# Performance work log

Hardware: AMD Instinct MI355X
Metric: run time of the kernel (lower is better)

Reference implementation:

```python
import jax, jax.numpy as jnp
import numpy as np
import math

B, C, H, W = 512, 64, 8, 8
E, NH, MEM = 64, 8, 8          # embed_dim, num_heads, mem_n
HD = E // NH                   # head_dim
THD = H * W * HD               # tot_head_dim = 512
AMB = 5.0                      # attn_mask_b
LN_EPS = 1e-5


def conv2d(x, w, b):
    y = jax.lax.conv_general_dilated(x, w, (1, 1), 'SAME',
                                     dimension_numbers=('NCHW', 'OIHW', 'NCHW'))
    return y + b[None, :, None, None]


def setup_inputs() -> dict:
    key = jax.random.key(0)
    ks = jax.random.split(key, 14)
    r = lambda k, s, sc=1.0: jax.random.normal(k, s, dtype=jnp.float32) * sc
    return {
        'input': r(ks[0], (B, C, H, W)),
        'h_cur': r(ks[1], (B, E, H, W)),
        'c_cur': r(ks[2], (B, E, H, W)),
        'concat_k': r(ks[3], (B, MEM, NH, THD)),
        'concat_v': r(ks[4], (B, MEM, NH, THD)),
        'attn_mask': jax.random.randint(ks[5], (B * NH, 1, MEM), 0, 2).astype(bool),
        'conv_w': r(ks[6], (5 * E, C + E, 3, 3), 0.05),
        'conv_b': jnp.zeros((5 * E,), jnp.float32),
        'proj_w': r(ks[7], (3 * E, C, 3, 3), 0.05),
        'proj_b': jnp.zeros((3 * E,), jnp.float32),
        'out_w': r(ks[8], (E, E, 3, 3), 0.05),
        'out_b': jnp.zeros((E,), jnp.float32),
        'ln_w': jnp.ones((E, H, W), jnp.float32),
        'ln_b': jnp.zeros((E, H, W), jnp.float32),
        'pos_w': r(ks[9], (MEM, H * W * E), 0.02),
        'pos_b': jax.random.uniform(ks[10], (MEM, NH), jnp.float32, -0.1, 0.1),
    }


def _cell(input, h_cur, c_cur, concat_k, concat_v, attn_mask,
          conv_w, conv_b, proj_w, proj_b, out_w, out_b, ln_w, ln_b, pos_w, pos_b):
    # ConvLSTM gates
    combined = jnp.concatenate([input, h_cur], axis=1)          # [B, C+E, H, W]
    cc = conv2d(combined, conv_w, conv_b)                       # [B, 5E, H, W]
    cc_i, cc_f, cc_o, cc_g, cc_a = jnp.split(cc, 5, axis=1)
    i = jax.nn.sigmoid(cc_i)
    f = jax.nn.sigmoid(cc_f)
    o = jax.nn.sigmoid(cc_o)
    g = jnp.tanh(cc_g)
    a = jax.nn.sigmoid(cc_a)
    c_next = f * c_cur + i * g

    # attention over growing memory
    kqv = conv2d(input, proj_w, proj_b)                         # [B, 3E, H, W]
    k, q, v = jnp.split(kqv, 3, axis=1)
    # [B, E, H, W] -> [B*NH, 1, THD] (contiguous split of E into NH heads)
    resh = lambda x: x.reshape(B * NH, 1, THD)
    k, q, v = resh(k), resh(q), resh(v)
    q_scaled = q / math.sqrt(THD)

    # prior memory: [B, MEM, NH, THD] -> [B*NH, MEM-1, THD]
    def mem_resh(m):
        return jnp.transpose(m[:, 1:], (1, 0, 2, 3)).reshape(MEM - 1, B * NH, THD).transpose(1, 0, 2)
    k_full = jnp.concatenate([mem_resh(concat_k), k], axis=1)   # [B*NH, MEM, THD]
    v_full = jnp.concatenate([mem_resh(concat_v), v], axis=1)

    # learned positional key offsets / score biases
    pos_w_e = jnp.broadcast_to(pos_w[:, None, :], (MEM, B, H * W * E)) \
                 .reshape(MEM, B * NH, THD).transpose(1, 0, 2)  # [B*NH, MEM, THD]
    pos_b_e = jnp.broadcast_to(pos_b[:, None, :], (MEM, B, NH)) \
                 .reshape(MEM, B * NH).T                        # [B*NH, MEM]
    k_full = k_full + pos_w_e

    # additive mask: -inf where masked, last slot forced to +attn_mask_b
    mask = jnp.where(attn_mask, -jnp.inf, 0.0).astype(q.dtype)  # [B*NH, 1, MEM]
    mask = mask.at[:, :, -1].set(AMB)

    scores = mask + jnp.einsum('bqd,bkd->bqk', q_scaled, k_full) + pos_b_e[:, None, :]
    w = jax.nn.softmax(scores, axis=-1)                         # [B*NH, 1, MEM]
    attn = jnp.einsum('bqk,bkd->bqd', w, v_full)                # [B*NH, 1, THD]
    attn = attn.reshape(B, E, H, W)

    out = conv2d(attn, out_w, out_b) + input[:, :E]
    # LayerNorm over (E, H, W)
    mu = jnp.mean(out, axis=(1, 2, 3), keepdims=True)
    var = jnp.mean((out - mu) ** 2, axis=(1, 2, 3), keepdims=True)
    out = (out - mu) / jnp.sqrt(var + LN_EPS) * ln_w[None] + ln_b[None]

    c_next = c_next + a * jnp.tanh(out)
    h_next = o * jnp.tanh(c_next)

    ret = lambda m: m.transpose(1, 0, 2).reshape(MEM, B, NH, THD).transpose(1, 0, 2, 3)
    return h_next, c_next, ret(k_full), ret(v_full)


def reference(input, h_cur, c_cur, concat_k, concat_v, attn_mask,
              conv_w, conv_b, proj_w, proj_b, out_w, out_b, ln_w, ln_b, pos_w, pos_b):
    return _cell(input, h_cur, c_cur, concat_k, concat_v, attn_mask,
                 conv_w, conv_b, proj_w, proj_b, out_w, out_b, ln_w, ln_b, pos_w, pos_b)
```

## Files before the change

kernel.cpp:

```cpp
#include <hip/hip_runtime.h>

typedef short short8 __attribute__((ext_vector_type(8)));
typedef __bf16 bf16x8 __attribute__((ext_vector_type(8)));
typedef float f32x4 __attribute__((ext_vector_type(4)));
typedef short s16x4 __attribute__((ext_vector_type(4)));
typedef unsigned u32x4 __attribute__((ext_vector_type(4)));

__device__ __forceinline__ short f2bf(float f) {
  unsigned u = __builtin_bit_cast(unsigned, f);
  u = (u + 0x7FFFu + ((u >> 16) & 1u)) >> 16;
  return (short)u;
}
__device__ __forceinline__ f32x4 mfma16(short8 a, short8 b, f32x4 c) {
  return __builtin_amdgcn_mfma_f32_16x16x32_bf16(
      __builtin_bit_cast(bf16x8, a), __builtin_bit_cast(bf16x8, b), c, 0, 0, 0);
}
__device__ __forceinline__ float sigm(float x) { return 1.0f / (1.0f + __expf(-x)); }
__device__ __forceinline__ float ftanh(float x) {
  return 1.0f - 2.0f / (1.0f + __expf(2.0f * x));
}
__device__ __forceinline__ f32x4 ntld4(const float* p) {
  return __builtin_nontemporal_load((const f32x4*)p);
}
__device__ __forceinline__ void ntst4(float* p, f32x4 v) {
  __builtin_nontemporal_store(v, (f32x4*)p);
}

__global__ void pack_w(const float* __restrict__ w1, const float* __restrict__ w2,
                       const float* __restrict__ w3, short* __restrict__ out) {
  int e = blockIdx.x * 256 + threadIdx.x;
  if (e < 46080) {
    int kb8 = e / 320, n = e % 320;
    short8 v;
#pragma unroll
    for (int j = 0; j < 8; ++j) {
      int k = kb8 * 8 + j;
      int tap = k >> 7, ci = k & 127;
      v[j] = f2bf(w1[(n * 128 + ci) * 9 + tap]);
    }
    *(short8*)&out[e * 8] = v;
    return;
  }
  e -= 46080;
  if (e < 13824) {
    int kb8 = e / 192, n = e % 192;
    short8 v;
#pragma unroll
    for (int j = 0; j < 8; ++j) {
      int k = kb8 * 8 + j;
      int tap = k >> 6, ci = k & 63;
      v[j] = f2bf(w2[(n * 64 + ci) * 9 + tap]);
    }
    *(short8*)&out[(46080 + e) * 8] = v;
    return;
  }
  e -= 13824;
  {
    int kb8 = e / 64, n = e % 64;
    short8 v;
#pragma unroll
    for (int j = 0; j < 8; ++j) {
      int k = kb8 * 8 + j;
      int tap = k >> 6, ci = k & 63;
      v[j] = f2bf(w3[(n * 64 + ci) * 9 + tap]);
    }
    *(short8*)&out[(46080 + 13824 + e) * 8] = v;
  }
}

__launch_bounds__(512, 4)
__global__ void mid_k(const float* __restrict__ input, const float* __restrict__ h_cur,
                      const float* __restrict__ c_cur, const float* __restrict__ ck,
                      const float* __restrict__ cv, const int* __restrict__ amask,
                      const float* __restrict__ conv_b, const float* __restrict__ proj_b,
                      const float* __restrict__ pos_w, const float* __restrict__ pos_b,
                      const short* __restrict__ pk1, const short* __restrict__ pk2,
                      float* __restrict__ o_k, float* __restrict__ o_v,
                      short* __restrict__ ws_attn, float* __restrict__ ws_ct,
                      unsigned* __restrict__ ws_oa) {
  __shared__ short comb[12800];
  __shared__ float Xb[4160];
  __shared__ float Vx[4160];
  __shared__ float sc_lds[8];
  float* combf = (float*)comb;
  unsigned* Xbu = (unsigned*)Xb;

  const int tid = threadIdx.x;
  const int wave = tid >> 6, lane = tid & 63;
  const int col = lane & 15, g4 = lane >> 4;
  const int wc = wave >> 1, wm = wave & 1;
  const int ch = wc * 16 + col;

  if (blockIdx.x < 512) {
    const int b = blockIdx.x;
    const int hd = wave;
    const int d0 = lane * 4, d1 = (lane + 64) * 4;
    if (tid < 8) sc_lds[tid] = 0.f;

#pragma unroll
    for (int i = 0; i < 2; ++i) {
      int idx = (tid + 512 * i) * 4;
      int c = idx >> 6, p0 = idx & 63;
      f32x4 vi = *(const f32x4*)&input[b * 4096 + idx];
#pragma unroll
      for (int j = 0; j < 4; ++j) {
        int p = p0 + j;
        int pp = ((p >> 3) + 1) * 10 + (p & 7) + 1;
        comb[pp * 64 + ((c + pp * 8) & 63)] = f2bf(vi[j]);
      }
    }
    for (int i = tid; i < 2304; i += 512) {
      int pr = i >> 6, c = i & 63;
      int pp = (pr < 10) ? pr
               : (pr < 20) ? (80 + pr)
               : (pr < 28) ? ((pr - 19) * 10)
                           : ((pr - 27) * 10 + 9);
      comb[pp * 64 + c] = 0;
    }
    __syncthreads();

    f32x4 acc2[2][3];
#pragma unroll
    for (int m = 0; m < 2; ++m)
#pragma unroll
      for (int g = 0; g < 3; ++g) acc2[m][g] = (f32x4){0.f, 0.f, 0.f, 0.f};
    short8 bb2[3];
#pragma unroll
    for (int g = 0; g < 3; ++g)
      bb2[g] = *(const short8*)&pk2[((g4)*192 + g * 64 + ch) * 8];
    for (int s = 0; s < 18; ++s) {
      short8 bbn[3];
      if (s < 17) {
        int kb8 = (s + 1) * 4 + g4;
#pragma unroll
        for (int g = 0; g < 3; ++g)
          bbn[g] = *(const short8*)&pk2[(kb8 * 192 + g * 64 + ch) * 8];
      }
      int tap = s >> 1, cib = s & 1;
      int kh = tap / 3, kw = tap % 3;
      short8 a[2];
#pragma unroll
      for (int m = 0; m < 2; ++m) {
        int p = (wm * 2 + m) * 16 + col;
        int pp = ((p >> 3) + kh) * 10 + (p & 7) + kw;
        int slot = (cib * 32 + g4 * 8 + pp * 8) & 63;
        a[m] = *(const short8*)&comb[pp * 64 + slot];
      }
#pragma unroll
      for (int m = 0; m < 2; ++m)
#pragma unroll
        for (int g = 0; g < 3; ++g) acc2[m][g] = mfma16(a[m], bb2[g], acc2[m][g]);
      if (s < 17) {
#pragma unroll
        for (int g = 0; g < 3; ++g) bb2[g] = bbn[g];
      }
    }

    float kreg[8], qreg[8], vreg[8], part7 = 0.f;
    {
      float pb0 = proj_b[ch], pb1 = proj_b[64 + ch], pb2 = proj_b[128 + ch];
      const float rsq = 0.044194173824159216f;
#pragma unroll
      for (int m = 0; m < 2; ++m)
#pragma unroll
        for (int r = 0; r < 4; ++r) {
          int p = (wm * 2 + m) * 16 + g4 * 4 + r;
          float kf = acc2[m][0][r] + pb0 + pos_w[7 * 4096 + ch * 64 + p];
          float qf = (acc2[m][1][r] + pb1) * rsq;
          float vf = acc2[m][2][r] + pb2;
          kreg[m * 4 + r] = kf;
          qreg[m * 4 + r] = qf;
          vreg[m * 4 + r] = vf;
          part7 = fmaf(qf, kf, part7);
        }
    }
    atomicAdd(&sc_lds[ch >> 3], part7);

    f32x4 kk0[7], kk1[7];
#pragma unroll
    for (int m = 0; m < 7; ++m) {
      const float* kp = ck + ((size_t)((b * 8 + m + 1) * 8 + hd)) * 512;
      kk0[m] = ntld4(kp + d0);
      kk1[m] = ntld4(kp + d1);
    }

    __syncthreads();

#pragma unroll
    for (int m = 0; m < 2; ++m)
#pragma unroll
      for (int r = 0; r < 4; ++r) {
        int p = (wm * 2 + m) * 16 + g4 * 4 + r;
        combf[ch * 65 + p] = kreg[m * 4 + r];
        Xb[ch * 65 + p] = qreg[m * 4 + r];
        Vx[ch * 65 + p] = vreg[m * 4 + r];
      }
    __syncthreads();

    const size_t base7 = (size_t)(b * 64 + 56) * 512;
#pragma unroll
    for (int i = 0; i < 2; ++i) {
      int idx = (tid + 512 * i) * 4;
      int c = idx >> 6, p0 = idx & 63;
      f32x4 kq, vq;
#pragma unroll
      for (int j = 0; j < 4; ++j) {
        kq[j] = combf[c * 65 + p0 + j];
        vq[j] = Vx[c * 65 + p0 + j];
      }
      ntst4(&o_k[base7 + idx], kq);
      ntst4(&o_v[base7 + idx], vq);
    }
    const int cs0 = d0 >> 6, po0 = d0 & 63, cs1 = d1 >> 6, po1 = d1 & 63;
    f32x4 q0, q1, v70, v71;
#pragma unroll
    for (int j = 0; j < 4; ++j) {
      q0[j] = Xb[(hd * 8 + cs0) * 65 + po0 + j];
      q1[j] = Xb[(hd * 8 + cs1) * 65 + po1 + j];
      v70[j] = Vx[(hd * 8 + cs0) * 65 + po0 + j];
      v71[j] = Vx[(hd * 8 + cs1) * 65 + po1 + j];
    }
    float sc7 = sc_lds[hd] + pos_b[7 * 8 + hd] + 5.0f;

    float scv[8];
    scv[7] = sc7;
#pragma unroll
    for (int m = 0; m < 7; ++m) {
      const float* pw = pos_w + m * 4096 + hd * 512;
      f32x4 k0 = kk0[m] + *(const f32x4*)&pw[d0];
      f32x4 k1 = kk1[m] + *(const f32x4*)&pw[d1];
      float* dst = o_k + ((size_t)((b * 8 + m) * 8 + hd)) * 512;
      ntst4(dst + d0, k0);
      ntst4(dst + d1, k1);
      float part = 0.f;
#pragma unroll
      for (int j = 0; j < 4; ++j) {
        part = fmaf(q0[j], k0[j], part);
        part = fmaf(q1[j], k1[j], part);
      }
#pragma unroll
      for (int off = 32; off >= 1; off >>= 1) part += __shfl_xor(part, off);
      float msk = amask[(b * 8 + hd) * 8 + m] ? -__builtin_inff() : 0.0f;
      scv[m] = part + pos_b[m * 8 + hd] + msk;
    }

    f32x4 vv0[7], vv1[7];
#pragma unroll
    for (int m = 0; m < 7; ++m) {
      const float* vp = cv + ((size_t)((b * 8 + m + 1) * 8 + hd)) * 512;
      vv0[m] = ntld4(vp + d0);
      vv1[m] = ntld4(vp + d1);
    }

    float mx = scv[0];
#pragma unroll
    for (int m = 1; m < 8; ++m) mx = fmaxf(mx, scv[m]);
    float w[8], s = 0.f;
#pragma unroll
    for (int m = 0; m < 8; ++m) {
      w[m] = __expf(scv[m] - mx);
      s += w[m];
    }
    float inv = 1.0f / s;
#pragma unroll
    for (int m = 0; m < 8; ++m) w[m] *= inv;

    f32x4 a0 = (f32x4){0.f, 0.f, 0.f, 0.f};
    f32x4 a1 = (f32x4){0.f, 0.f, 0.f, 0.f};
#pragma unroll
    for (int m = 0; m < 7; ++m) {
      float* dst = o_v + ((size_t)((b * 8 + m) * 8 + hd)) * 512;
      ntst4(dst + d0, vv0[m]);
      ntst4(dst + d1, vv1[m]);
      a0 += vv0[m] * w[m];
      a1 += vv1[m] * w[m];
    }
    a0 += v70 * w[7];
    a1 += v71 * w[7];

    s16x4 s0, s1;
#pragma unroll
    for (int j = 0; j < 4; ++j) {
      s0[j] = f2bf(a0[j]);
      s1[j] = f2bf(a1[j]);
    }
    *(s16x4*)&ws_attn[(size_t)b * 4096 + hd * 512 + d0] = s0;
    *(s16x4*)&ws_attn[(size_t)b * 4096 + hd * 512 + d1] = s1;
  } else {
    const int b = blockIdx.x - 512;
#pragma unroll
    for (int i = 0; i < 2; ++i) {
      int idx = (tid + 512 * i) * 4;
      int c = idx >> 6, p0 = idx & 63;
      f32x4 vi = *(const f32x4*)&input[b * 4096 + idx];
      f32x4 vh = *(const f32x4*)&h_cur[b * 4096 + idx];
      f32x4 vc = *(const f32x4*)&c_cur[b * 4096 + idx];
#pragma unroll
      for (int j = 0; j < 4; ++j) {
        int p = p0 + j;
        int pp = ((p >> 3) + 1) * 10 + (p & 7) + 1;
        comb[pp * 128 + ((c + pp * 8) & 127)] = f2bf(vi[j]);
        comb[pp * 128 + ((c + 64 + pp * 8) & 127)] = f2bf(vh[j]);
        Xb[c * 65 + p] = vc[j];
      }
    }
    for (int i = tid; i < 4608; i += 512) {
      int pr = i >> 7, c = i & 127;
      int pp = (pr < 10) ? pr
               : (pr < 20) ? (80 + pr)
               : (pr < 28) ? ((pr - 19) * 10)
                           : ((pr - 27) * 10 + 9);
      comb[pp * 128 + c] = 0;
    }
    __syncthreads();

    f32x4 acc1[2][5];
#pragma unroll
    for (int m = 0; m < 2; ++m)
#pragma unroll
      for (int g = 0; g < 5; ++g) acc1[m][g] = (f32x4){0.f, 0.f, 0.f, 0.f};
    short8 bb1[5];
#pragma unroll
    for (int g = 0; g < 5; ++g)
      bb1[g] = *(const short8*)&pk1[((g4)*320 + g * 64 + ch) * 8];
    for (int s = 0; s < 36; ++s) {
      short8 bbn[5];
      if (s < 35) {
        int kb8 = (s + 1) * 4 + g4;
#pragma unroll
        for (int g = 0; g < 5; ++g)
          bbn[g] = *(const short8*)&pk1[(kb8 * 320 + g * 64 + ch) * 8];
      }
      int tap = s >> 2, cib = s & 3;
      int kh = tap / 3, kw = tap % 3;
      short8 a[2];
#pragma unroll
      for (int m = 0; m < 2; ++m) {
        int p = (wm * 2 + m) * 16 + col;
        int pp = ((p >> 3) + kh) * 10 + (p & 7) + kw;
        int slot = (cib * 32 + g4 * 8 + pp * 8) & 127;
        a[m] = *(const short8*)&comb[pp * 128 + slot];
      }
#pragma unroll
      for (int m = 0; m < 2; ++m)
#pragma unroll
        for (int g = 0; g < 5; ++g) acc1[m][g] = mfma16(a[m], bb1[g], acc1[m][g]);
      if (s < 35) {
#pragma unroll
        for (int g = 0; g < 5; ++g) bb1[g] = bbn[g];
      }
    }

    float ctv[8];
    unsigned oav[8];
    {
      float bi0 = conv_b[ch], bi1 = conv_b[64 + ch], bi2 = conv_b[128 + ch];
      float bi3 = conv_b[192 + ch], bi4 = conv_b[256 + ch];
#pragma unroll
      for (int m = 0; m < 2; ++m)
#pragma unroll
        for (int r = 0; r < 4; ++r) {
          int p = (wm * 2 + m) * 16 + g4 * 4 + r;
          float iv = sigm(acc1[m][0][r] + bi0);
          float fv = sigm(acc1[m][1][r] + bi1);
          float ov = sigm(acc1[m][2][r] + bi2);
          float gv = ftanh(acc1[m][3][r] + bi3);
          float av = sigm(acc1[m][4][r] + bi4);
          ctv[m * 4 + r] = fv * Xb[ch * 65 + p] + iv * gv;
          oav[m * 4 + r] = ((unsigned)(unsigned short)f2bf(av) << 16) |
                           (unsigned)(unsigned short)f2bf(ov);
        }
    }
    __syncthreads();
#pragma unroll
    for (int m = 0; m < 2; ++m)
#pragma unroll
      for (int r = 0; r < 4; ++r) {
        int p = (wm * 2 + m) * 16 + g4 * 4 + r;
        combf[ch * 65 + p] = ctv[m * 4 + r];
        Xbu[ch * 65 + p] = oav[m * 4 + r];
      }
    __syncthreads();
#pragma unroll
    for (int i = 0; i < 2; ++i) {
      int idx = (tid + 512 * i) * 4;
      int c = idx >> 6, p0 = idx & 63;
      f32x4 cq;
      u32x4 oq;
#pragma unroll
      for (int j = 0; j < 4; ++j) {
        cq[j] = combf[c * 65 + p0 + j];
        oq[j] = Xbu[c * 65 + p0 + j];
      }
      *(f32x4*)&ws_ct[(size_t)b * 4096 + idx] = cq;
      *(u32x4*)&ws_oa[(size_t)b * 4096 + idx] = oq;
    }
  }
}

__launch_bounds__(512, 4)
__global__ void back_k(const float* __restrict__ input,
                       const short* __restrict__ ws_attn,
                       const float* __restrict__ ws_ct,
                       const unsigned* __restrict__ ws_oa,
                       const float* __restrict__ out_b,
                       const float* __restrict__ ln_w, const float* __restrict__ ln_b,
                       const short* __restrict__ pk3,
                       float* __restrict__ o_h, float* __restrict__ o_c) {
  __shared__ short comb[8320];
  __shared__ float Xb[4160];
  __shared__ float red[16];
  float* combf = (float*)comb;
  unsigned* Xbu = (unsigned*)Xb;

  const int b = blockIdx.x;
  const int tid = threadIdx.x;
  const int wave = tid >> 6, lane = tid & 63;
  const int col = lane & 15, g4 = lane >> 4;
  const int wc = wave >> 1, wm = wave & 1;
  const int ch = wc * 16 + col;

  f32x4 ctr[2];
  u32x4 oar[2];
#pragma unroll
  for (int i = 0; i < 2; ++i) {
    int idx = (tid + 512 * i) * 4;
    ctr[i] = *(const f32x4*)&ws_ct[(size_t)b * 4096 + idx];
    oar[i] = *(const u32x4*)&ws_oa[(size_t)b * 4096 + idx];
  }
#pragma unroll
  for (int i = 0; i < 2; ++i) {
    int idx = (tid + 512 * i) * 4;
    int c = idx >> 6, p0 = idx & 63;
    s16x4 av = *(const s16x4*)&ws_attn[(size_t)b * 4096 + idx];
    f32x4 vi = *(const f32x4*)&input[b * 4096 + idx];
#pragma unroll
    for (int j = 0; j < 4; ++j) {
      int p = p0 + j;
      int pp = ((p >> 3) + 1) * 10 + (p & 7) + 1;
      comb[pp * 64 + ((c + pp * 8) & 63)] = av[j];
      Xb[c * 65 + p] = vi[j];
    }
  }
  for (int i = tid; i < 2304; i += 512) {
    int pr = i >> 6, c = i & 63;
    int pp = (pr < 10) ? pr
             : (pr < 20) ? (80 + pr)
             : (pr < 28) ? ((pr - 19) * 10)
                         : ((pr - 27) * 10 + 9);
    comb[pp * 64 + c] = 0;
  }
  __syncthreads();

  f32x4 acc3[2];
  acc3[0] = (f32x4){0.f, 0.f, 0.f, 0.f};
  acc3[1] = (f32x4){0.f, 0.f, 0.f, 0.f};
  short8 bb3 = *(const short8*)&pk3[((g4)*64 + ch) * 8];
  for (int s = 0; s < 18; ++s) {
    short8 bbn;
    if (s < 17) {
      int kb8 = (s + 1) * 4 + g4;
      bbn = *(const short8*)&pk3[(kb8 * 64 + ch) * 8];
    }
    int tap = s >> 1, cib = s & 1;
    int kh = tap / 3, kw = tap % 3;
    short8 a[2];
#pragma unroll
    for (int m = 0; m < 2; ++m) {
      int p = (wm * 2 + m) * 16 + col;
      int pp = ((p >> 3) + kh) * 10 + (p & 7) + kw;
      int slot = (cib * 32 + g4 * 8 + pp * 8) & 63;
      a[m] = *(const short8*)&comb[pp * 64 + slot];
    }
#pragma unroll
    for (int m = 0; m < 2; ++m) acc3[m] = mfma16(a[m], bb3, acc3[m]);
    if (s < 17) bb3 = bbn;
  }

  float ov_[8], s1 = 0.f, s2 = 0.f;
  {
    float ob = out_b[ch];
#pragma unroll
    for (int m = 0; m < 2; ++m)
#pragma unroll
      for (int r = 0; r < 4; ++r) {
        int p = (wm * 2 + m) * 16 + g4 * 4 + r;
        float v = acc3[m][r] + ob + Xb[ch * 65 + p];
        ov_[m * 4 + r] = v;
        s1 += v;
        s2 += v * v;
      }
  }
#pragma unroll
  for (int off = 32; off >= 1; off >>= 1) {
    s1 += __shfl_xor(s1, off);
    s2 += __shfl_xor(s2, off);
  }
  if (lane == 0) { red[wave] = s1; red[8 + wave] = s2; }
  __syncthreads();
  float ts1 = 0.f, ts2 = 0.f;
#pragma unroll
  for (int w = 0; w < 8; ++w) { ts1 += red[w]; ts2 += red[8 + w]; }
  float mu = ts1 * (1.0f / 4096.0f);
  float var = ts2 * (1.0f / 4096.0f) - mu * mu;
  float rstd = rsqrtf(var + 1e-5f);

#pragma unroll
  for (int i = 0; i < 2; ++i) {
    int idx = (tid + 512 * i) * 4;
    int c = idx >> 6, p0 = idx & 63;
#pragma unroll
    for (int j = 0; j < 4; ++j) {
      combf[c * 65 + p0 + j] = ctr[i][j];
      Xbu[c * 65 + p0 + j] = oar[i][j];
    }
  }
  __syncthreads();

#pragma unroll
  for (int m = 0; m < 2; ++m)
#pragma unroll
    for (int r = 0; r < 4; ++r) {
      int p = (wm * 2 + m) * 16 + g4 * 4 + r;
      float ct = combf[ch * 65 + p];
      unsigned u = Xbu[ch * 65 + p];
      float og = __builtin_bit_cast(float, u << 16);
      float ag = __builtin_bit_cast(float, u & 0xffff0000u);
      float oln = (ov_[m * 4 + r] - mu) * rstd * ln_w[ch * 64 + p] + ln_b[ch * 64 + p];
      float cn = ct + ag * ftanh(oln);
      float hv = og * ftanh(cn);
      combf[ch * 65 + p] = hv;
      Xb[ch * 65 + p] = cn;
    }
  __syncthreads();
#pragma unroll
  for (int i = 0; i < 2; ++i) {
    int idx = (tid + 512 * i) * 4;
    int c = idx >> 6, p0 = idx & 63;
    f32x4 hq, cq;
#pragma unroll
    for (int j = 0; j < 4; ++j) {
      hq[j] = combf[c * 65 + p0 + j];
      cq[j] = Xb[c * 65 + p0 + j];
    }
    *(f32x4*)&o_h[b * 4096 + idx] = hq;
    *(f32x4*)&o_c[b * 4096 + idx] = cq;
  }
}

__launch_bounds__(512, 4)
__global__ void kqv_k(const float* __restrict__ input,
                      const float* __restrict__ proj_b,
                      const float* __restrict__ pos_w,
                      const short* __restrict__ pk2,
                      float* __restrict__ q_out, float* __restrict__ o_k,
                      float* __restrict__ o_v) {
  __shared__ short comb[6400];
  __shared__ float Xk[4160], Xq[4160], Xv[4160];
  const int b = blockIdx.x;
  const int tid = threadIdx.x;
  const int wave = tid >> 6, lane = tid & 63;
  const int col = lane & 15, g4 = lane >> 4;
  const int wc = wave >> 1, wm = wave & 1;
  const int ch = wc * 16 + col;
#pragma unroll
  for (int i = 0; i < 2; ++i) {
    int idx = (tid + 512 * i) * 4;
    int c = idx >> 6, p0 = idx & 63;
    f32x4 vi = *(const f32x4*)&input[b * 4096 + idx];
#pragma unroll
    for (int j = 0; j < 4; ++j) {
      int p = p0 + j;
      int pp = ((p >> 3) + 1) * 10 + (p & 7) + 1;
      comb[pp * 64 + ((c + pp * 8) & 63)] = f2bf(vi[j]);
    }
  }
  for (int i = tid; i < 2304; i += 512) {
    int pr = i >> 6, c = i & 63;
    int pp = (pr < 10) ? pr
             : (pr < 20) ? (80 + pr)
             : (pr < 28) ? ((pr - 19) * 10)
                         : ((pr - 27) * 10 + 9);
    comb[pp * 64 + c] = 0;
  }
  __syncthreads();
  f32x4 acc2[2][3];
#pragma unroll
  for (int m = 0; m < 2; ++m)
#pragma unroll
    for (int g = 0; g < 3; ++g) acc2[m][g] = (f32x4){0.f, 0.f, 0.f, 0.f};
  short8 bb2[3];
#pragma unroll
  for (int g = 0; g < 3; ++g)
    bb2[g] = *(const short8*)&pk2[((g4)*192 + g * 64 + ch) * 8];
  for (int s = 0; s < 18; ++s) {
    short8 bbn[3];
    if (s < 17) {
      int kb8 = (s + 1) * 4 + g4;
#pragma unroll
      for (int g = 0; g < 3; ++g)
        bbn[g] = *(const short8*)&pk2[(kb8 * 192 + g * 64 + ch) * 8];
    }
    int tap = s >> 1, cib = s & 1;
    int kh = tap / 3, kw = tap % 3;
    short8 a[2];
#pragma unroll
    for (int m = 0; m < 2; ++m) {
      int p = (wm * 2 + m) * 16 + col;
      int pp = ((p >> 3) + kh) * 10 + (p & 7) + kw;
      int slot = (cib * 32 + g4 * 8 + pp * 8) & 63;
      a[m] = *(const short8*)&comb[pp * 64 + slot];
    }
#pragma unroll
    for (int m = 0; m < 2; ++m)
#pragma unroll
      for (int g = 0; g < 3; ++g) acc2[m][g] = mfma16(a[m], bb2[g], acc2[m][g]);
    if (s < 17) {
#pragma unroll
      for (int g = 0; g < 3; ++g) bb2[g] = bbn[g];
    }
  }
  {
    float pb0 = proj_b[ch], pb1 = proj_b[64 + ch], pb2 = proj_b[128 + ch];
    const float rsq = 0.044194173824159216f;
#pragma unroll
    for (int m = 0; m < 2; ++m)
#pragma unroll
      for (int r = 0; r < 4; ++r) {
        int p = (wm * 2 + m) * 16 + g4 * 4 + r;
        Xk[ch * 65 + p] = acc2[m][0][r] + pb0 + pos_w[7 * 4096 + ch * 64 + p];
        Xq[ch * 65 + p] = (acc2[m][1][r] + pb1) * rsq;
        Xv[ch * 65 + p] = acc2[m][2][r] + pb2;
      }
  }
  __syncthreads();
  const size_t base7 = (size_t)(b * 64 + 56) * 512;
#pragma unroll
  for (int i = 0; i < 2; ++i) {
    int idx = (tid + 512 * i) * 4;
    int c = idx >> 6, p0 = idx & 63;
    f32x4 kq, qq, vq;
#pragma unroll
    for (int j = 0; j < 4; ++j) {
      kq[j] = Xk[c * 65 + p0 + j];
      qq[j] = Xq[c * 65 + p0 + j];
      vq[j] = Xv[c * 65 + p0 + j];
    }
    *(f32x4*)&o_k[base7 + idx] = kq;
    *(f32x4*)&q_out[(size_t)b * 4096 + idx] = qq;
    *(f32x4*)&o_v[base7 + idx] = vq;
  }
}

__launch_bounds__(64, 4)
__global__ void attn_k(const float* __restrict__ ck, const float* __restrict__ cv,
                       const int* __restrict__ amask,
                       const float* __restrict__ pos_w,
                       const float* __restrict__ pos_b,
                       const float* __restrict__ q_in,
                       float* __restrict__ o_k, float* __restrict__ o_v,
                       float* __restrict__ attn_out) {
  const int b = blockIdx.x >> 3;
  const int hd = blockIdx.x & 7;
  const int lane = threadIdx.x;
  const int d0 = lane * 4, d1 = (lane + 64) * 4;
  const float* qp = q_in + (size_t)b * 4096 + hd * 512;
  f32x4 q0 = *(const f32x4*)&qp[d0];
  f32x4 q1 = *(const f32x4*)&qp[d1];
  float sc[8];
#pragma unroll
  for (int m = 0; m < 7; ++m) {
    const float* kp = ck + ((size_t)((b * 8 + m + 1) * 8 + hd)) * 512;
    const float* pw = pos_w + m * 4096 + hd * 512;
    f32x4 k0 = ntld4(kp + d0) + *(const f32x4*)&pw[d0];
    f32x4 k1 = ntld4(kp + d1) + *(const f32x4*)&pw[d1];
    float* dst = o_k + ((size_t)((b * 8 + m) * 8 + hd)) * 512;
    ntst4(dst + d0, k0);
    ntst4(dst + d1, k1);
    float part = 0.f;
#pragma unroll
    for (int j = 0; j < 4; ++j) {
      part = fmaf(q0[j], k0[j], part);
      part = fmaf(q1[j], k1[j], part);
    }
#pragma unroll
    for (int off = 32; off >= 1; off >>= 1) part += __shfl_xor(part, off);
    float msk = amask[(b * 8 + hd) * 8 + m] ? -__builtin_inff() : 0.0f;
    sc[m] = part + pos_b[m * 8 + hd] + msk;
  }
  {
    const float* kp = o_k + ((size_t)((b * 8 + 7) * 8 + hd)) * 512;
    f32x4 k0 = *(const f32x4*)&kp[d0];
    f32x4 k1 = *(const f32x4*)&kp[d1];
    float part = 0.f;
#pragma unroll
    for (int j = 0; j < 4; ++j) {
      part = fmaf(q0[j], k0[j], part);
      part = fmaf(q1[j], k1[j], part);
    }
#pragma unroll
    for (int off = 32; off >= 1; off >>= 1) part += __shfl_xor(part, off);
    sc[7] = part + pos_b[7 * 8 + hd] + 5.0f;
  }
  float mx = sc[0];
#pragma unroll
  for (int m = 1; m < 8; ++m) mx = fmaxf(mx, sc[m]);
  float w[8], s = 0.f;
#pragma unroll
  for (int m = 0; m < 8; ++m) {
    w[m] = __expf(sc[m] - mx);
    s += w[m];
  }
  float inv = 1.0f / s;
#pragma unroll
  for (int m = 0; m < 8; ++m) w[m] *= inv;
  f32x4 a0 = (f32x4){0.f, 0.f, 0.f, 0.f};
  f32x4 a1 = (f32x4){0.f, 0.f, 0.f, 0.f};
#pragma unroll
  for (int m = 0; m < 7; ++m) {
    const float* vp = cv + ((size_t)((b * 8 + m + 1) * 8 + hd)) * 512;
    f32x4 v0 = ntld4(vp + d0);
    f32x4 v1 = ntld4(vp + d1);
    float* dst = o_v + ((size_t)((b * 8 + m) * 8 + hd)) * 512;
    ntst4(dst + d0, v0);
    ntst4(dst + d1, v1);
    a0 += v0 * w[m];
    a1 += v1 * w[m];
  }
  {
    const float* vp = o_v + ((size_t)((b * 8 + 7) * 8 + hd)) * 512;
    a0 += *(const f32x4*)&vp[d0] * w[7];
    a1 += *(const f32x4*)&vp[d1] * w[7];
  }
  float* ap = attn_out + (size_t)b * 4096 + hd * 512;
  *(f32x4*)&ap[d0] = a0;
  *(f32x4*)&ap[d1] = a1;
}

__launch_bounds__(512, 4)
__global__ void cell2_k(
    const float* __restrict__ input, const float* __restrict__ h_cur,
    const float* __restrict__ c_cur, const float* __restrict__ attn_in,
    const float* __restrict__ conv_b, const float* __restrict__ out_b,
    const float* __restrict__ ln_w, const float* __restrict__ ln_b,
    const short* __restrict__ pk1, const short* __restrict__ pk3,
    float* __restrict__ o_h, float* __restrict__ o_c) {
  __shared__ short comb[12800];
  __shared__ float Xb[4160];
  __shared__ float Qb[4160];
  __shared__ float Vb[4160];
  __shared__ float red[16];
  const int b = blockIdx.x;
  const int tid = threadIdx.x;
  const int wave = tid >> 6, lane = tid & 63;
  const int col = lane & 15, g4 = lane >> 4;
  const int wc = wave >> 1, wm = wave & 1;
  const int ch = wc * 16 + col;
#pragma unroll
  for (int i = 0; i < 2; ++i) {
    int idx = (tid + 512 * i) * 4;
    int c = idx >> 6, p0 = idx & 63;
    f32x4 vi = *(const f32x4*)&input[b * 4096 + idx];
    f32x4 vh = *(const f32x4*)&h_cur[b * 4096 + idx];
    f32x4 vc = *(const f32x4*)&c_cur[b * 4096 + idx];
#pragma unroll
    for (int j = 0; j < 4; ++j) {
      int p = p0 + j;
      int pp = ((p >> 3) + 1) * 10 + (p & 7) + 1;
      comb[pp * 128 + ((c + pp * 8) & 127)] = f2bf(vi[j]);
      comb[pp * 128 + ((c + 64 + pp * 8) & 127)] = f2bf(vh[j]);
      Xb[c * 65 + p] = vc[j];
    }
  }
  for (int i = tid; i < 4608; i += 512) {
    int pr = i >> 7, c = i & 127;
    int pp = (pr < 10) ? pr
             : (pr < 20) ? (80 + pr)
             : (pr < 28) ? ((pr - 19) * 10)
                         : ((pr - 27) * 10 + 9);
    comb[pp * 128 + c] = 0;
  }
  __syncthreads();
  f32x4 acc1[2][5];
#pragma unroll
  for (int m = 0; m < 2; ++m)
#pragma unroll
    for (int g = 0; g < 5; ++g) acc1[m][g] = (f32x4){0.f, 0.f, 0.f, 0.f};
  short8 bb1[5];
#pragma unroll
  for (int g = 0; g < 5; ++g)
    bb1[g] = *(const short8*)&pk1[((g4)*320 + g * 64 + ch) * 8];
  for (int s = 0; s < 36; ++s) {
    short8 bbn[5];
    if (s < 35) {
      int kb8 = (s + 1) * 4 + g4;
#pragma unroll
      for (int g = 0; g < 5; ++g)
        bbn[g] = *(const short8*)&pk1[(kb8 * 320 + g * 64 + ch) * 8];
    }
    int tap = s >> 2, cib = s & 3;
    int kh = tap / 3, kw = tap % 3;
    short8 a[2];
#pragma unroll
    for (int m = 0; m < 2; ++m) {
      int p = (wm * 2 + m) * 16 + col;
      int pp = ((p >> 3) + kh) * 10 + (p & 7) + kw;
      int slot = (cib * 32 + g4 * 8 + pp * 8) & 127;
      a[m] = *(const short8*)&comb[pp * 128 + slot];
    }
#pragma unroll
    for (int m = 0; m < 2; ++m)
#pragma unroll
      for (int g = 0; g < 5; ++g) acc1[m][g] = mfma16(a[m], bb1[g], acc1[m][g]);
    if (s < 35) {
#pragma unroll
      for (int g = 0; g < 5; ++g) bb1[g] = bbn[g];
    }
  }
  float ct_r[8], o_r[8], a_r[8];
  {
    float bi0 = conv_b[ch], bi1 = conv_b[64 + ch], bi2 = conv_b[128 + ch];
    float bi3 = conv_b[192 + ch], bi4 = conv_b[256 + ch];
#pragma unroll
    for (int m = 0; m < 2; ++m)
#pragma unroll
      for (int r = 0; r < 4; ++r) {
        int p = (wm * 2 + m) * 16 + g4 * 4 + r;
        float iv = sigm(acc1[m][0][r] + bi0);
        float fv = sigm(acc1[m][1][r] + bi1);
        float ov = sigm(acc1[m][2][r] + bi2);
        float gv = ftanh(acc1[m][3][r] + bi3);
        float av = sigm(acc1[m][4][r] + bi4);
        ct_r[m * 4 + r] = fv * Xb[ch * 65 + p] + iv * gv;
        o_r[m * 4 + r] = ov;
        a_r[m * 4 + r] = av;
      }
  }
  __syncthreads();
  {
    f32x4 av[2], iv[2];
#pragma unroll
    for (int i = 0; i < 2; ++i) {
      int idx = (tid + 512 * i) * 4;
      av[i] = *(const f32x4*)&attn_in[b * 4096 + idx];
      iv[i] = *(const f32x4*)&input[b * 4096 + idx];
    }
#pragma unroll
    for (int i = 0; i < 2; ++i) {
      int idx = (tid + 512 * i) * 4;
      int c = idx >> 6, p0 = idx & 63;
#pragma unroll
      for (int j = 0; j < 4; ++j) {
        int p = p0 + j;
        int pp = ((p >> 3) + 1) * 10 + (p & 7) + 1;
        comb[pp * 128 + ((c + pp * 8) & 127)] = f2bf(av[i][j]);
        Xb[c * 65 + p] = iv[i][j];
      }
    }
  }
  __syncthreads();
  f32x4 acc3[2];
  acc3[0] = (f32x4){0.f, 0.f, 0.f, 0.f};
  acc3[1] = (f32x4){0.f, 0.f, 0.f, 0.f};
  short8 bb3 = *(const short8*)&pk3[((g4)*64 + ch) * 8];
  for (int s = 0; s < 18; ++s) {
    short8 bbn;
    if (s < 17) {
      int kb8 = (s + 1) * 4 + g4;
      bbn = *(const short8*)&pk3[(kb8 * 64 + ch) * 8];
    }
    int tap = s >> 1, cib = s & 1;
    int kh = tap / 3, kw = tap % 3;
    short8 a[2];
#pragma unroll
    for (int m = 0; m < 2; ++m) {
      int p = (wm * 2 + m) * 16 + col;
      int pp = ((p >> 3) + kh) * 10 + (p & 7) + kw;
      int slot = (cib * 32 + g4 * 8 + pp * 8) & 127;
      a[m] = *(const short8*)&comb[pp * 128 + slot];
    }
#pragma unroll
    for (int m = 0; m < 2; ++m) acc3[m] = mfma16(a[m], bb3, acc3[m]);
    if (s < 17) bb3 = bbn;
  }
  float ov_[8], s1 = 0.f, s2 = 0.f;
  {
    float ob = out_b[ch];
#pragma unroll
    for (int m = 0; m < 2; ++m)
#pragma unroll
      for (int r = 0; r < 4; ++r) {
        int p = (wm * 2 + m) * 16 + g4 * 4 + r;
        float v = acc3[m][r] + ob + Xb[ch * 65 + p];
        ov_[m * 4 + r] = v;
        s1 += v;
        s2 += v * v;
      }
  }
#pragma unroll
  for (int off = 32; off >= 1; off >>= 1) {
    s1 += __shfl_xor(s1, off);
    s2 += __shfl_xor(s2, off);
  }
  if (lane == 0) { red[wave] = s1; red[8 + wave] = s2; }
  __syncthreads();
  float ts1 = 0.f, ts2 = 0.f;
#pragma unroll
  for (int w = 0; w < 8; ++w) { ts1 += red[w]; ts2 += red[8 + w]; }
  float mu = ts1 * (1.0f / 4096.0f);
  float var = ts2 * (1.0f / 4096.0f) - mu * mu;
  float rstd = rsqrtf(var + 1e-5f);
#pragma unroll
  for (int m = 0; m < 2; ++m)
#pragma unroll
    for (int r = 0; r < 4; ++r) {
      int p = (wm * 2 + m) * 16 + g4 * 4 + r;
      float oln = (ov_[m * 4 + r] - mu) * rstd * ln_w[ch * 64 + p] + ln_b[ch * 64 + p];
      float cn = ct_r[m * 4 + r] + a_r[m * 4 + r] * ftanh(oln);
      float hv = o_r[m * 4 + r] * ftanh(cn);
      Qb[ch * 65 + p] = hv;
      Vb[ch * 65 + p] = cn;
    }
  __syncthreads();
#pragma unroll
  for (int i = 0; i < 2; ++i) {
    int idx = (tid + 512 * i) * 4;
    int c = idx >> 6, p0 = idx & 63;
    f32x4 hv, cvv;
#pragma unroll
    for (int j = 0; j < 4; ++j) {
      hv[j] = Qb[c * 65 + p0 + j];
      cvv[j] = Vb[c * 65 + p0 + j];
    }
    *(f32x4*)&o_h[b * 4096 + idx] = hv;
    *(f32x4*)&o_c[b * 4096 + idx] = cvv;
  }
}

extern "C" void kernel_launch(void* const* d_in, const int* in_sizes, int n_in,
                              void* d_out, int out_size, void* d_ws, size_t ws_size,
                              hipStream_t stream) {
  (void)in_sizes; (void)n_in; (void)out_size;
  const float* input  = (const float*)d_in[0];
  const float* h_cur  = (const float*)d_in[1];
  const float* c_cur  = (const float*)d_in[2];
  const float* ck     = (const float*)d_in[3];
  const float* cv     = (const float*)d_in[4];
  const int*   amask  = (const int*)d_in[5];
  const float* conv_w = (const float*)d_in[6];
  const float* conv_b = (const float*)d_in[7];
  const float* proj_w = (const float*)d_in[8];
  const float* proj_b = (const float*)d_in[9];
  const float* out_w  = (const float*)d_in[10];
  const float* out_b  = (const float*)d_in[11];
  const float* ln_w   = (const float*)d_in[12];
  const float* ln_b   = (const float*)d_in[13];
  const float* pos_w  = (const float*)d_in[14];
  const float* pos_b  = (const float*)d_in[15];

  char* ws = (char*)d_ws;
  short* pk = (short*)ws;
  float* o_h = (float*)d_out;
  float* o_c = o_h + 2097152;
  float* o_k = o_h + 4194304;
  float* o_v = o_h + 20971520;

  pack_w<<<252, 256, 0, stream>>>(conv_w, proj_w, out_w, pk);

  if (ws_size >= (24u << 20)) {
    short* ws_attn = (short*)(ws + (2u << 20));
    float* ws_ct = (float*)(ws + (8u << 20));
    unsigned* ws_oa = (unsigned*)(ws + (16u << 20));
    mid_k<<<1024, 512, 0, stream>>>(input, h_cur, c_cur, ck, cv, amask,
                                    conv_b, proj_b, pos_w, pos_b,
                                    pk, pk + 368640,
                                    o_k, o_v, ws_attn, ws_ct, ws_oa);
    back_k<<<512, 512, 0, stream>>>(input, ws_attn, ws_ct, ws_oa,
                                    out_b, ln_w, ln_b, pk + 479232, o_h, o_c);
  } else {
    kqv_k<<<512, 512, 0, stream>>>(input, proj_b, pos_w, pk + 368640,
                                   o_h, o_k, o_v);
    attn_k<<<4096, 64, 0, stream>>>(ck, cv, amask, pos_w, pos_b, o_h,
                                    o_k, o_v, o_c);
    cell2_k<<<512, 512, 0, stream>>>(input, h_cur, c_cur, o_c,
                                     conv_b, out_b, ln_w, ln_b,
                                     pk, pk + 479232, o_h, o_c);
  }
}
```

Measured before the change: 106.0 us.

## Move V-weighted sum and V copy into tail kernel, pass softmax weights

The attention-weighted sum over V, and the copy of concat_v into the output, move from the mid kernel to the tail kernel. The mid kernel now writes only the normalized softmax weights per head to workspace, which lowers its register pressure and load traffic and balances work between the two kernels. Nontemporal loads are replaced with plain loads throughout, and the position-7 V store becomes a regular store so the tail kernel can read it back. The tail kernel then does extra global loads and scatters the bf16 attention result into LDS itself.

Result: faster. 99.34 us (-6.3%).

```diff
diff --git a/kernel.cpp b/kernel.cpp
--- a/kernel.cpp
+++ b/kernel.cpp
@@ -19,9 +19,7 @@
 __device__ __forceinline__ float ftanh(float x) {
   return 1.0f - 2.0f / (1.0f + __expf(2.0f * x));
 }
-__device__ __forceinline__ f32x4 ntld4(const float* p) {
-  return __builtin_nontemporal_load((const f32x4*)p);
-}
+__device__ __forceinline__ f32x4 ld4(const float* p) { return *(const f32x4*)p; }
 __device__ __forceinline__ void ntst4(float* p, f32x4 v) {
   __builtin_nontemporal_store(v, (f32x4*)p);
 }
@@ -69,15 +67,15 @@
 }
 
 __launch_bounds__(512, 4)
-__global__ void mid_k(const float* __restrict__ input, const float* __restrict__ h_cur,
-                      const float* __restrict__ c_cur, const float* __restrict__ ck,
-                      const float* __restrict__ cv, const int* __restrict__ amask,
-                      const float* __restrict__ conv_b, const float* __restrict__ proj_b,
-                      const float* __restrict__ pos_w, const float* __restrict__ pos_b,
-                      const short* __restrict__ pk1, const short* __restrict__ pk2,
-                      float* __restrict__ o_k, float* __restrict__ o_v,
-                      short* __restrict__ ws_attn, float* __restrict__ ws_ct,
-                      unsigned* __restrict__ ws_oa) {
+__global__ void mid2_k(const float* __restrict__ input, const float* __restrict__ h_cur,
+                       const float* __restrict__ c_cur, const float* __restrict__ ck,
+                       const int* __restrict__ amask,
+                       const float* __restrict__ conv_b, const float* __restrict__ proj_b,
+                       const float* __restrict__ pos_w, const float* __restrict__ pos_b,
+                       const short* __restrict__ pk1, const short* __restrict__ pk2,
+                       float* __restrict__ o_k, float* __restrict__ o_v,
+                       float* __restrict__ ws_wt, float* __restrict__ ws_ct,
+                       unsigned* __restrict__ ws_oa) {
   __shared__ short comb[12800];
   __shared__ float Xb[4160];
   __shared__ float Vx[4160];
@@ -101,7 +99,7 @@
     for (int i = 0; i < 2; ++i) {
       int idx = (tid + 512 * i) * 4;
       int c = idx >> 6, p0 = idx & 63;
-      f32x4 vi = *(const f32x4*)&input[b * 4096 + idx];
+      f32x4 vi = ld4(&input[b * 4096 + idx]);
 #pragma unroll
       for (int j = 0; j < 4; ++j) {
         int p = p0 + j;
@@ -176,12 +174,12 @@
     }
     atomicAdd(&sc_lds[ch >> 3], part7);
 
-    f32x4 kk0[7], kk1[7];
+    int msks[7];
+    float pbv[7];
 #pragma unroll
     for (int m = 0; m < 7; ++m) {
-      const float* kp = ck + ((size_t)((b * 8 + m + 1) * 8 + hd)) * 512;
-      kk0[m] = ntld4(kp + d0);
-      kk1[m] = ntld4(kp + d1);
+      msks[m] = amask[(b * 8 + hd) * 8 + m];
+      pbv[m] = pos_b[m * 8 + hd];
     }
 
     __syncthreads();
@@ -209,16 +207,14 @@
         vq[j] = Vx[c * 65 + p0 + j];
       }
       ntst4(&o_k[base7 + idx], kq);
-      ntst4(&o_v[base7 + idx], vq);
+      *(f32x4*)&o_v[base7 + idx] = vq;
     }
     const int cs0 = d0 >> 6, po0 = d0 & 63, cs1 = d1 >> 6, po1 = d1 & 63;
-    f32x4 q0, q1, v70, v71;
+    f32x4 q0, q1;
 #pragma unroll
     for (int j = 0; j < 4; ++j) {
       q0[j] = Xb[(hd * 8 + cs0) * 65 + po0 + j];
       q1[j] = Xb[(hd * 8 + cs1) * 65 + po1 + j];
-      v70[j] = Vx[(hd * 8 + cs0) * 65 + po0 + j];
-      v71[j] = Vx[(hd * 8 + cs1) * 65 + po1 + j];
     }
     float sc7 = sc_lds[hd] + pos_b[7 * 8 + hd] + 5.0f;
 
@@ -226,9 +222,10 @@
     scv[7] = sc7;
 #pragma unroll
     for (int m = 0; m < 7; ++m) {
+      const float* kp = ck + ((size_t)((b * 8 + m + 1) * 8 + hd)) * 512;
       const float* pw = pos_w + m * 4096 + hd * 512;
-      f32x4 k0 = kk0[m] + *(const f32x4*)&pw[d0];
-      f32x4 k1 = kk1[m] + *(const f32x4*)&pw[d1];
+      f32x4 k0 = ld4(kp + d0) + ld4(pw + d0);
+      f32x4 k1 = ld4(kp + d1) + ld4(pw + d1);
       float* dst = o_k + ((size_t)((b * 8 + m) * 8 + hd)) * 512;
       ntst4(dst + d0, k0);
       ntst4(dst + d1, k1);
@@ -240,16 +237,7 @@
       }
 #pragma unroll
       for (int off = 32; off >= 1; off >>= 1) part += __shfl_xor(part, off);
-      float msk = amask[(b * 8 + hd) * 8 + m] ? -__builtin_inff() : 0.0f;
-      scv[m] = part + pos_b[m * 8 + hd] + msk;
-    }
-
-    f32x4 vv0[7], vv1[7];
-#pragma unroll
-    for (int m = 0; m < 7; ++m) {
-      const float* vp = cv + ((size_t)((b * 8 + m + 1) * 8 + hd)) * 512;
-      vv0[m] = ntld4(vp + d0);
-      vv1[m] = ntld4(vp + d1);
+      scv[m] = part + pbv[m] + (msks[m] ? -__builtin_inff() : 0.0f);
     }
 
     float mx = scv[0];
@@ -262,39 +250,20 @@
       s += w[m];
     }
     float inv = 1.0f / s;
-#pragma unroll
-    for (int m = 0; m < 8; ++m) w[m] *= inv;
-
-    f32x4 a0 = (f32x4){0.f, 0.f, 0.f, 0.f};
-    f32x4 a1 = (f32x4){0.f, 0.f, 0.f, 0.f};
-#pragma unroll
-    for (int m = 0; m < 7; ++m) {
-      float* dst = o_v + ((size_t)((b * 8 + m) * 8 + hd)) * 512;
-      ntst4(dst + d0, vv0[m]);
-      ntst4(dst + d1, vv1[m]);
-      a0 += vv0[m] * w[m];
-      a1 += vv1[m] * w[m];
-    }
-    a0 += v70 * w[7];
-    a1 += v71 * w[7];
-
-    s16x4 s0, s1;
-#pragma unroll
-    for (int j = 0; j < 4; ++j) {
-      s0[j] = f2bf(a0[j]);
-      s1[j] = f2bf(a1[j]);
-    }
-    *(s16x4*)&ws_attn[(size_t)b * 4096 + hd * 512 + d0] = s0;
-    *(s16x4*)&ws_attn[(size_t)b * 4096 + hd * 512 + d1] = s1;
+    if (lane == 0) {
+#pragma unroll
+      for (int m = 0; m < 8; ++m)
+        ws_wt[(size_t)b * 64 + hd * 8 + m] = w[m] * inv;
+    }
   } else {
     const int b = blockIdx.x - 512;
 #pragma unroll
     for (int i = 0; i < 2; ++i) {
       int idx = (tid + 512 * i) * 4;
       int c = idx >> 6, p0 = idx & 63;
-      f32x4 vi = *(const f32x4*)&input[b * 4096 + idx];
-      f32x4 vh = *(const f32x4*)&h_cur[b * 4096 + idx];
-      f32x4 vc = *(const f32x4*)&c_cur[b * 4096 + idx];
+      f32x4 vi = ld4(&input[b * 4096 + idx]);
+      f32x4 vh = ld4(&h_cur[b * 4096 + idx]);
+      f32x4 vc = ld4(&c_cur[b * 4096 + idx]);
 #pragma unroll
       for (int j = 0; j < 4; ++j) {
         int p = p0 + j;
@@ -399,16 +368,18 @@
 }
 
 __launch_bounds__(512, 4)
-__global__ void back_k(const float* __restrict__ input,
-                       const short* __restrict__ ws_attn,
+__global__ void tail_k(const float* __restrict__ input, const float* __restrict__ cv,
+                       const float* __restrict__ ws_wt,
                        const float* __restrict__ ws_ct,
                        const unsigned* __restrict__ ws_oa,
                        const float* __restrict__ out_b,
                        const float* __restrict__ ln_w, const float* __restrict__ ln_b,
                        const short* __restrict__ pk3,
-                       float* __restrict__ o_h, float* __restrict__ o_c) {
+                       float* __restrict__ o_h, float* __restrict__ o_c,
+                       float* __restrict__ o_v) {
   __shared__ short comb[8320];
   __shared__ float Xb[4160];
+  __shared__ float wt_s[64];
   __shared__ float red[16];
   float* combf = (float*)comb;
   unsigned* Xbu = (unsigned*)Xb;
@@ -419,28 +390,26 @@
   const int col = lane & 15, g4 = lane >> 4;
   const int wc = wave >> 1, wm = wave & 1;
   const int ch = wc * 16 + col;
+  const int hd = wave;
+  const int d0 = lane * 4, d1 = (lane + 64) * 4;
 
   f32x4 ctr[2];
   u32x4 oar[2];
 #pragma unroll
   for (int i = 0; i < 2; ++i) {
     int idx = (tid + 512 * i) * 4;
-    ctr[i] = *(const f32x4*)&ws_ct[(size_t)b * 4096 + idx];
+    ctr[i] = ld4(&ws_ct[(size_t)b * 4096 + idx]);
     oar[i] = *(const u32x4*)&ws_oa[(size_t)b * 4096 + idx];
   }
+  if (tid < 64) wt_s[tid] = ws_wt[(size_t)b * 64 + tid];
+
 #pragma unroll
   for (int i = 0; i < 2; ++i) {
     int idx = (tid + 512 * i) * 4;
     int c = idx >> 6, p0 = idx & 63;
-    s16x4 av = *(const s16x4*)&ws_attn[(size_t)b * 4096 + idx];
-    f32x4 vi = *(const f32x4*)&input[b * 4096 + idx];
-#pragma unroll
-    for (int j = 0; j < 4; ++j) {
-      int p = p0 + j;
-      int pp = ((p >> 3) + 1) * 10 + (p & 7) + 1;
-      comb[pp * 64 + ((c + pp * 8) & 63)] = av[j];
-      Xb[c * 65 + p] = vi[j];
-    }
+    f32x4 vi = ld4(&input[b * 4096 + idx]);
+#pragma unroll
+    for (int j = 0; j < 4; ++j) Xb[c * 65 + p0 + j] = vi[j];
   }
   for (int i = tid; i < 2304; i += 512) {
     int pr = i >> 6, c = i & 63;
@@ -449,6 +418,40 @@
              : (pr < 28) ? ((pr - 19) * 10)
                          : ((pr - 27) * 10 + 9);
     comb[pp * 64 + c] = 0;
+  }
+  __syncthreads();
+
+  float wv[8];
+#pragma unroll
+  for (int m = 0; m < 8; ++m) wv[m] = wt_s[hd * 8 + m];
+
+  f32x4 a0 = (f32x4){0.f, 0.f, 0.f, 0.f};
+  f32x4 a1 = (f32x4){0.f, 0.f, 0.f, 0.f};
+#pragma unroll
+  for (int m = 0; m < 7; ++m) {
+    const float* vp = cv + ((size_t)((b * 8 + m + 1) * 8 + hd)) * 512;
+    f32x4 v0 = ld4(vp + d0);
+    f32x4 v1 = ld4(vp + d1);
+    float* dst = o_v + ((size_t)((b * 8 + m) * 8 + hd)) * 512;
+    ntst4(dst + d0, v0);
+    ntst4(dst + d1, v1);
+    a0 += v0 * wv[m];
+    a1 += v1 * wv[m];
+  }
+  {
+    const float* vp = o_v + ((size_t)((b * 8 + 7) * 8 + hd)) * 512;
+    a0 += ld4(vp + d0) * wv[7];
+    a1 += ld4(vp + d1) * wv[7];
+  }
+#pragma unroll
+  for (int j = 0; j < 4; ++j) {
+    int dA = d0 + j, dB = d1 + j;
+    int cA = hd * 8 + (dA >> 6), pA = dA & 63;
+    int cB = hd * 8 + (dB >> 6), pB = dB & 63;
+    int ppA = ((pA >> 3) + 1) * 10 + (pA & 7) + 1;
+    int ppB = ((pB >> 3) + 1) * 10 + (pB & 7) + 1;
+    comb[ppA * 64 + ((cA + ppA * 8) & 63)] = f2bf(a0[j]);
+    comb[ppB * 64 + ((cB + ppB * 8) & 63)] = f2bf(a1[j]);
   }
   __syncthreads();
 
@@ -567,7 +570,7 @@
   for (int i = 0; i < 2; ++i) {
     int idx = (tid + 512 * i) * 4;
     int c = idx >> 6, p0 = idx & 63;
-    f32x4 vi = *(const f32x4*)&input[b * 4096 + idx];
+    f32x4 vi = ld4(&input[b * 4096 + idx]);
 #pragma unroll
     for (int j = 0; j < 4; ++j) {
       int p = p0 + j;
@@ -665,15 +668,15 @@
   const int lane = threadIdx.x;
   const int d0 = lane * 4, d1 = (lane + 64) * 4;
   const float* qp = q_in + (size_t)b * 4096 + hd * 512;
-  f32x4 q0 = *(const f32x4*)&qp[d0];
-  f32x4 q1 = *(const f32x4*)&qp[d1];
+  f32x4 q0 = ld4(qp + d0);
+  f32x4 q1 = ld4(qp + d1);
   float sc[8];
 #pragma unroll
   for (int m = 0; m < 7; ++m) {
     const float* kp = ck + ((size_t)((b * 8 + m + 1) * 8 + hd)) * 512;
     const float* pw = pos_w + m * 4096 + hd * 512;
-    f32x4 k0 = ntld4(kp + d0) + *(const f32x4*)&pw[d0];
-    f32x4 k1 = ntld4(kp + d1) + *(const f32x4*)&pw[d1];
+    f32x4 k0 = ld4(kp + d0) + ld4(pw + d0);
+    f32x4 k1 = ld4(kp + d1) + ld4(pw + d1);
     float* dst = o_k + ((size_t)((b * 8 + m) * 8 + hd)) * 512;
     ntst4(dst + d0, k0);
     ntst4(dst + d1, k1);
@@ -690,8 +693,8 @@
   }
   {
     const float* kp = o_k + ((size_t)((b * 8 + 7) * 8 + hd)) * 512;
-    f32x4 k0 = *(const f32x4*)&kp[d0];
-    f32x4 k1 = *(const f32x4*)&kp[d1];
+    f32x4 k0 = ld4(kp + d0);
+    f32x4 k1 = ld4(kp + d1);
     float part = 0.f;
 #pragma unroll
     for (int j = 0; j < 4; ++j) {
@@ -719,8 +722,8 @@
 #pragma unroll
   for (int m = 0; m < 7; ++m) {
     const float* vp = cv + ((size_t)((b * 8 + m + 1) * 8 + hd)) * 512;
-    f32x4 v0 = ntld4(vp + d0);
-    f32x4 v1 = ntld4(vp + d1);
+    f32x4 v0 = ld4(vp + d0);
+    f32x4 v1 = ld4(vp + d1);
     float* dst = o_v + ((size_t)((b * 8 + m) * 8 + hd)) * 512;
     ntst4(dst + d0, v0);
     ntst4(dst + d1, v1);
@@ -729,8 +732,8 @@
   }
   {
     const float* vp = o_v + ((size_t)((b * 8 + 7) * 8 + hd)) * 512;
-    a0 += *(const f32x4*)&vp[d0] * w[7];
-    a1 += *(const f32x4*)&vp[d1] * w[7];
+    a0 += ld4(vp + d0) * w[7];
+    a1 += ld4(vp + d1) * w[7];
   }
   float* ap = attn_out + (size_t)b * 4096 + hd * 512;
   *(f32x4*)&ap[d0] = a0;
@@ -760,9 +763,9 @@
   for (int i = 0; i < 2; ++i) {
     int idx = (tid + 512 * i) * 4;
     int c = idx >> 6, p0 = idx & 63;
-    f32x4 vi = *(const f32x4*)&input[b * 4096 + idx];
-    f32x4 vh = *(const f32x4*)&h_cur[b * 4096 + idx];
-    f32x4 vc = *(const f32x4*)&c_cur[b * 4096 + idx];
+    f32x4 vi = ld4(&input[b * 4096 + idx]);
+    f32x4 vh = ld4(&h_cur[b * 4096 + idx]);
+    f32x4 vc = ld4(&c_cur[b * 4096 + idx]);
 #pragma unroll
     for (int j = 0; j < 4; ++j) {
       int p = p0 + j;
@@ -842,8 +845,8 @@
 #pragma unroll
     for (int i = 0; i < 2; ++i) {
       int idx = (tid + 512 * i) * 4;
-      av[i] = *(const f32x4*)&attn_in[b * 4096 + idx];
-      iv[i] = *(const f32x4*)&input[b * 4096 + idx];
+      av[i] = ld4(&attn_in[b * 4096 + idx]);
+      iv[i] = ld4(&input[b * 4096 + idx]);
     }
 #pragma unroll
     for (int i = 0; i < 2; ++i) {
@@ -968,15 +971,16 @@
   pack_w<<<252, 256, 0, stream>>>(conv_w, proj_w, out_w, pk);
 
   if (ws_size >= (24u << 20)) {
-    short* ws_attn = (short*)(ws + (2u << 20));
+    float* ws_wt = (float*)(ws + (2u << 20));
     float* ws_ct = (float*)(ws + (8u << 20));
     unsigned* ws_oa = (unsigned*)(ws + (16u << 20));
-    mid_k<<<1024, 512, 0, stream>>>(input, h_cur, c_cur, ck, cv, amask,
-                                    conv_b, proj_b, pos_w, pos_b,
-                                    pk, pk + 368640,
-                                    o_k, o_v, ws_attn, ws_ct, ws_oa);
-    back_k<<<512, 512, 0, stream>>>(input, ws_attn, ws_ct, ws_oa,
-                                    out_b, ln_w, ln_b, pk + 479232, o_h, o_c);
+    mid2_k<<<1024, 512, 0, stream>>>(input, h_cur, c_cur, ck, amask,
+                                     conv_b, proj_b, pos_w, pos_b,
+                                     pk, pk + 368640,
+                                     o_k, o_v, ws_wt, ws_ct, ws_oa);
+    tail_k<<<512, 512, 0, stream>>>(input, cv, ws_wt, ws_ct, ws_oa,
+                                    out_b, ln_w, ln_b, pk + 479232,
+                                    o_h, o_c, o_v);
   } else {
     kqv_k<<<512, 512, 0, stream>>>(input, proj_b, pos_w, pk + 368640,
                                    o_h, o_k, o_v);
```
